# Performance work log

Hardware: AMD Instinct MI355X
Metric: run time of the kernel (lower is better)

## Reference

```python
import jax, jax.numpy as jnp
import numpy as np


def setup_inputs() -> dict:
    key = jax.random.key(0)
    k1, k2 = jax.random.split(key)
    B, C, H, W = 4, 256, 64, 64
    kernel_size, ratio = 5, 2
    x = jax.random.normal(k1, (B, C, H, W), dtype=jnp.float32)
    kernel = jax.random.uniform(k2, (B, kernel_size ** 2, H * ratio, W * ratio), dtype=jnp.float32)
    return {"x": x, "kernel": kernel, "kernel_size": kernel_size, "ratio": ratio}


def reference(x, kernel, kernel_size, ratio):
    # x: [B, C, H, W]; kernel: [B, k^2, H*ratio, W*ratio]
    B, C, H, W = x.shape
    pad = kernel_size // 2  # original hardcodes padding=2 for k=5
    xp = jnp.pad(x, ((0, 0), (0, 0), (pad, pad), (pad, pad)))
    # unfold: patches[b, ki*k+kj, c, h, w] = xp[b, c, h+ki, w+kj]
    patches = jnp.stack(
        [xp[:, :, i:i + H, j:j + W] for i in range(kernel_size) for j in range(kernel_size)],
        axis=1,
    )  # [B, k2, C, H, W]
    k2 = kernel_size ** 2
    # out[b,c,h*r+p,w*r+q] = sum_k patches[b,k,c,h,w] * kernel[b,k,h*r+p,w*r+q]
    kr = kernel.reshape(B, k2, H, ratio, W, ratio)
    out = jnp.einsum('bkchw,bkhpwq->bchpwq', patches, kr)
    return out.reshape(B, C, H * ratio, W * ratio)
```

## Files before the change

### kernel.cpp

```cpp
#include <hip/hip_runtime.h>


typedef float v4 __attribute__((ext_vector_type(4)));

__global__ __launch_bounds__(256, 2)
void carafe_kernel(const float* __restrict__ x,
                   const float* __restrict__ kern,
                   float* __restrict__ out) {
    __shared__ __align__(16) float wt[25 * 256];

    const int raw = blockIdx.x;
    const int l   = (raw & 7) * 128 + (raw >> 3);
    const int cc  = l & 3;
    const int h   = (l >> 2) & 63;
    const int b   = l >> 8;
    const int tid = threadIdx.x;
    const int t   = tid & 15;
    const int g   = tid >> 4;
    const int c0  = cc * 64 + g * 4;

    const float* kbase = kern + (size_t)b * 25 * 16384 + (size_t)(2 * h) * 128;
    const int stid = tid ^ (((tid >> 6) & 1) << 2);
#pragma unroll
    for (int i = 0; i < 25; ++i)
        wt[i * 256 + stid] = kbase[(size_t)i * 16384 + tid];
    __syncthreads();

    float acc[4][4][2][2] = {};

    const float* xb  = x + (size_t)(b * 256 + c0) * 4096;
    const int    wsw = (t >= 8) ? 4 : 0;

#pragma unroll
    for (int ki = 0; ki < 5; ++ki) {
        const int gr = h + ki - 2;
        if ((unsigned)gr >= 64u) continue;

        float xw[4][9];
#pragma unroll
        for (int ch = 0; ch < 4; ++ch) {
            const float* rowp = xb + (size_t)ch * 4096 + gr * 64;
            const v4 A  = *(const v4*)(rowp + (t ? 4 * t - 4 : 0));
            const v4 Bv = *(const v4*)(rowp + 4 * t);
            const v4 D  = *(const v4*)(rowp + (t < 15 ? 4 * t + 4 : 60));
            xw[ch][0] = t ? A.z : 0.0f;
            xw[ch][1] = t ? A.w : 0.0f;
            xw[ch][2] = Bv.x; xw[ch][3] = Bv.y; xw[ch][4] = Bv.z; xw[ch][5] = Bv.w;
            xw[ch][6] = (t < 15) ? D.x : 0.0f;
            xw[ch][7] = (t < 15) ? D.y : 0.0f;
            xw[ch][8] = (t < 15) ? D.z : 0.0f;
        }

#pragma unroll
        for (int kj = 0; kj < 5; ++kj) {
            const int k  = ki * 5 + kj;
            const int f0 = k * 256 + 8 * t;
            const int f1 = f0 + 128;
            const v4 w0a = *(const v4*)&wt[f0 ^ wsw];
            const v4 w0b = *(const v4*)&wt[(f0 + 4) ^ wsw];
            const v4 w1a = *(const v4*)&wt[f1 ^ wsw];
            const v4 w1b = *(const v4*)&wt[(f1 + 4) ^ wsw];
            const float w0v[8] = {w0a.x, w0a.y, w0a.z, w0a.w, w0b.x, w0b.y, w0b.z, w0b.w};
            const float w1v[8] = {w1a.x, w1a.y, w1a.z, w1a.w, w1b.x, w1b.y, w1b.z, w1b.w};
#pragma unroll
            for (int ch = 0; ch < 4; ++ch) {
#pragma unroll
                for (int cj = 0; cj < 4; ++cj) {
                    const float xv = xw[ch][cj + kj];
                    acc[ch][cj][0][0] += w0v[2 * cj]     * xv;
                    acc[ch][cj][0][1] += w0v[2 * cj + 1] * xv;
                    acc[ch][cj][1][0] += w1v[2 * cj]     * xv;
                    acc[ch][cj][1][1] += w1v[2 * cj + 1] * xv;
                }
            }
        }
    }

#pragma unroll
    for (int ch = 0; ch < 4; ++ch) {
        float* ob = out + ((size_t)(b * 256 + c0 + ch) * 128 + 2 * h) * 128 + 8 * t;
#pragma unroll
        for (int p = 0; p < 2; ++p) {
            v4 s0, s1;
            s0.x = acc[ch][0][p][0]; s0.y = acc[ch][0][p][1];
            s0.z = acc[ch][1][p][0]; s0.w = acc[ch][1][p][1];
            s1.x = acc[ch][2][p][0]; s1.y = acc[ch][2][p][1];
            s1.z = acc[ch][3][p][0]; s1.w = acc[ch][3][p][1];
            *(v4*)(ob + p * 128)     = s0;
            *(v4*)(ob + p * 128 + 4) = s1;
        }
    }
}

extern "C" void kernel_launch(void* const* d_in, const int* in_sizes, int n_in,
                              void* d_out, int out_size, void* d_ws, size_t ws_size,
                              hipStream_t stream) {
    const float* x    = (const float*)d_in[0];
    const float* kern = (const float*)d_in[1];
    float* out        = (float*)d_out;
    carafe_kernel<<<dim3(1024), dim3(256), 0, stream>>>(x, kern, out);
}
```

Before: 30.84 us.

## Halve per-thread output tile and double grid to raise occupancy

Each thread now computes 2 input columns (4 output columns) instead of 4, with 32 threads per row and 32 channels per block. The grid doubles to 2048 blocks and launch bounds target 4 blocks per SM. The shared-memory swizzle is removed in favour of plain float4 reads. The goal is more occupancy and parallelism to hide memory latency. The cost is that each block reloads the 25x256 weight tile for half as many channels, doubling weight traffic, and x halo reuse per thread drops.

```diff
diff --git a/kernel.cpp b/kernel.cpp
--- a/kernel.cpp
+++ b/kernel.cpp
@@ -1,76 +1,67 @@
 #include <hip/hip_runtime.h>
 
 
+typedef float v2 __attribute__((ext_vector_type(2)));
 typedef float v4 __attribute__((ext_vector_type(4)));
 
-__global__ __launch_bounds__(256, 2)
+__global__ __launch_bounds__(256, 4)
 void carafe_kernel(const float* __restrict__ x,
                    const float* __restrict__ kern,
                    float* __restrict__ out) {
     __shared__ __align__(16) float wt[25 * 256];
 
     const int raw = blockIdx.x;
-    const int l   = (raw & 7) * 128 + (raw >> 3);
-    const int cc  = l & 3;
-    const int h   = (l >> 2) & 63;
-    const int b   = l >> 8;
+    const int l   = (raw & 7) * 256 + (raw >> 3);
+    const int cc  = l & 7;
+    const int h   = (l >> 3) & 63;
+    const int b   = l >> 9;
     const int tid = threadIdx.x;
-    const int t   = tid & 15;
-    const int g   = tid >> 4;
-    const int c0  = cc * 64 + g * 4;
+    const int t   = tid & 31;
+    const int g   = tid >> 5;
+    const int c0  = cc * 32 + g * 4;
 
     const float* kbase = kern + (size_t)b * 25 * 16384 + (size_t)(2 * h) * 128;
-    const int stid = tid ^ (((tid >> 6) & 1) << 2);
 #pragma unroll
     for (int i = 0; i < 25; ++i)
-        wt[i * 256 + stid] = kbase[(size_t)i * 16384 + tid];
+        wt[i * 256 + tid] = kbase[(size_t)i * 16384 + tid];
     __syncthreads();
 
-    float acc[4][4][2][2] = {};
-
-    const float* xb  = x + (size_t)(b * 256 + c0) * 4096;
-    const int    wsw = (t >= 8) ? 4 : 0;
+    float acc[4][2][2][2] = {};
+    const float* xb = x + (size_t)(b * 256 + c0) * 4096;
 
 #pragma unroll
     for (int ki = 0; ki < 5; ++ki) {
         const int gr = h + ki - 2;
         if ((unsigned)gr >= 64u) continue;
 
-        float xw[4][9];
+        float xw[4][6];
 #pragma unroll
         for (int ch = 0; ch < 4; ++ch) {
             const float* rowp = xb + (size_t)ch * 4096 + gr * 64;
-            const v4 A  = *(const v4*)(rowp + (t ? 4 * t - 4 : 0));
-            const v4 Bv = *(const v4*)(rowp + 4 * t);
-            const v4 D  = *(const v4*)(rowp + (t < 15 ? 4 * t + 4 : 60));
-            xw[ch][0] = t ? A.z : 0.0f;
-            xw[ch][1] = t ? A.w : 0.0f;
-            xw[ch][2] = Bv.x; xw[ch][3] = Bv.y; xw[ch][4] = Bv.z; xw[ch][5] = Bv.w;
-            xw[ch][6] = (t < 15) ? D.x : 0.0f;
-            xw[ch][7] = (t < 15) ? D.y : 0.0f;
-            xw[ch][8] = (t < 15) ? D.z : 0.0f;
+            const v2 A = *(const v2*)(rowp + (t ? 2 * t - 2 : 0));
+            const v2 B = *(const v2*)(rowp + 2 * t);
+            const v2 C = *(const v2*)(rowp + (t < 31 ? 2 * t + 2 : 60));
+            xw[ch][0] = t ? A.x : 0.0f;
+            xw[ch][1] = t ? A.y : 0.0f;
+            xw[ch][2] = B.x;  xw[ch][3] = B.y;
+            xw[ch][4] = (t < 31) ? C.x : 0.0f;
+            xw[ch][5] = (t < 31) ? C.y : 0.0f;
         }
 
 #pragma unroll
         for (int kj = 0; kj < 5; ++kj) {
-            const int k  = ki * 5 + kj;
-            const int f0 = k * 256 + 8 * t;
-            const int f1 = f0 + 128;
-            const v4 w0a = *(const v4*)&wt[f0 ^ wsw];
-            const v4 w0b = *(const v4*)&wt[(f0 + 4) ^ wsw];
-            const v4 w1a = *(const v4*)&wt[f1 ^ wsw];
-            const v4 w1b = *(const v4*)&wt[(f1 + 4) ^ wsw];
-            const float w0v[8] = {w0a.x, w0a.y, w0a.z, w0a.w, w0b.x, w0b.y, w0b.z, w0b.w};
-            const float w1v[8] = {w1a.x, w1a.y, w1a.z, w1a.w, w1b.x, w1b.y, w1b.z, w1b.w};
+            const int k = ki * 5 + kj;
+            const v4 w0 = *(const v4*)&wt[k * 256 + 4 * t];
+            const v4 w1 = *(const v4*)&wt[k * 256 + 128 + 4 * t];
 #pragma unroll
             for (int ch = 0; ch < 4; ++ch) {
 #pragma unroll
-                for (int cj = 0; cj < 4; ++cj) {
+                for (int cj = 0; cj < 2; ++cj) {
                     const float xv = xw[ch][cj + kj];
-                    acc[ch][cj][0][0] += w0v[2 * cj]     * xv;
-                    acc[ch][cj][0][1] += w0v[2 * cj + 1] * xv;
-                    acc[ch][cj][1][0] += w1v[2 * cj]     * xv;
-                    acc[ch][cj][1][1] += w1v[2 * cj + 1] * xv;
+                    acc[ch][cj][0][0] += w0[2 * cj]     * xv;
+                    acc[ch][cj][0][1] += w0[2 * cj + 1] * xv;
+                    acc[ch][cj][1][0] += w1[2 * cj]     * xv;
+                    acc[ch][cj][1][1] += w1[2 * cj + 1] * xv;
                 }
             }
         }
@@ -78,16 +69,13 @@
 
 #pragma unroll
     for (int ch = 0; ch < 4; ++ch) {
-        float* ob = out + ((size_t)(b * 256 + c0 + ch) * 128 + 2 * h) * 128 + 8 * t;
+        float* ob = out + ((size_t)(b * 256 + c0 + ch) * 128 + 2 * h) * 128 + 4 * t;
 #pragma unroll
         for (int p = 0; p < 2; ++p) {
-            v4 s0, s1;
-            s0.x = acc[ch][0][p][0]; s0.y = acc[ch][0][p][1];
-            s0.z = acc[ch][1][p][0]; s0.w = acc[ch][1][p][1];
-            s1.x = acc[ch][2][p][0]; s1.y = acc[ch][2][p][1];
-            s1.z = acc[ch][3][p][0]; s1.w = acc[ch][3][p][1];
-            *(v4*)(ob + p * 128)     = s0;
-            *(v4*)(ob + p * 128 + 4) = s1;
+            v4 s;
+            s.x = acc[ch][0][p][0]; s.y = acc[ch][0][p][1];
+            s.z = acc[ch][1][p][0]; s.w = acc[ch][1][p][1];
+            *(v4*)(ob + p * 128) = s;
         }
     }
 }
@@ -98,5 +86,5 @@
     const float* x    = (const float*)d_in[0];
     const float* kern = (const float*)d_in[1];
     float* out        = (float*)d_out;
-    carafe_kernel<<<dim3(1024), dim3(256), 0, stream>>>(x, kern, out);
+    carafe_kernel<<<dim3(2048), dim3(256), 0, stream>>>(x, kern, out);
 }
```

Measured after the change: 29.27 us. 1.05x faster.
